# Kernel tuning notes

Hardware: AMD Instinct MI355X
Metric: run time of the kernel (lower is better)

## Reference

```python
import jax, jax.numpy as jnp
import numpy as np

# config (from LLObjectCondensation defaults)
Q_MIN = 0.5
S_B = 1.0
POT_SCALE = 1.0
REP_SCALE = 1.0
BETA_SCALE = 1.0
K_MAX = 128  # max objects per event; truth id 0 == noise


def setup_inputs() -> dict:
    key = jax.random.key(0)
    k1, k2, k3 = jax.random.split(key, 3)
    B, N, C = 8, 40000, 2
    ccoords = jax.random.normal(k1, (B, N, C), dtype=jnp.float32)
    beta = jax.random.uniform(k2, (B, N), dtype=jnp.float32, minval=1e-3, maxval=1.0 - 1e-3)
    t_idx = jax.random.randint(k3, (B, N), 0, K_MAX, dtype=jnp.int32)
    return {"ccoords": ccoords, "beta": beta, "t_idx": t_idx}


def reference(ccoords, beta, t_idx):
    B, N, C = ccoords.shape
    K = K_MAX
    beta_c = jnp.clip(beta, 1e-6, 1.0 - 1e-5)
    # charge q = arctanh^2(beta) + q_min
    q = jnp.arctanh(beta_c / 1.002) ** 2 + Q_MIN  # [B,N]

    obj_ids = jnp.arange(K, dtype=t_idx.dtype)
    M = t_idx[:, :, None] == obj_ids  # [B,N,K] hit-belongs-to-object mask
    is_noise = t_idx == 0  # [B,N]
    obj_present = jnp.any(M, axis=1) & (obj_ids > 0)  # [B,K]

    # condensation point alpha_k = argmax beta among hits of object k
    beta_m = jnp.where(M, beta_c[:, :, None], -1.0)  # [B,N,K]
    alpha = jnp.argmax(beta_m, axis=1)  # [B,K]
    x_alpha = jnp.take_along_axis(
        ccoords, jnp.broadcast_to(alpha[:, :, None], (B, K, C)), axis=1
    )  # [B,K,C]
    q_alpha = jnp.take_along_axis(q, alpha, axis=1)  # [B,K]
    beta_alpha = jnp.take_along_axis(beta_c, alpha, axis=1)  # [B,K]

    # pairwise squared distances hit <-> condensation point, via GEMM form
    xn2 = jnp.sum(ccoords * ccoords, axis=-1)  # [B,N]
    xa2 = jnp.sum(x_alpha * x_alpha, axis=-1)  # [B,K]
    d2 = xn2[:, :, None] + xa2[:, None, :] - 2.0 * jnp.einsum(
        "bnc,bkc->bnk", ccoords, x_alpha
    )
    d2 = jnp.maximum(d2, 0.0)
    d = jnp.sqrt(d2 + 1e-6)

    qq = q[:, :, None] * q_alpha[:, None, :]  # [B,N,K]
    pm = obj_present[:, None, :]
    # attractive: same-object hits pulled to condensation point
    V_attr = jnp.sum(jnp.where(M & pm, d2 * qq, 0.0), axis=(1, 2)) / N  # [B]
    # repulsive: other hits pushed away inside unit radius (hinge)
    V_rep = jnp.sum(
        jnp.where((~M) & pm, jnp.maximum(0.0, 1.0 - d) * qq, 0.0), axis=(1, 2)
    ) / N  # [B]

    n_obj = jnp.maximum(jnp.sum(obj_present, axis=-1), 1)
    L_beta = jnp.sum(jnp.where(obj_present, 1.0 - beta_alpha, 0.0), axis=-1) / n_obj
    n_noise = jnp.maximum(jnp.sum(is_noise, axis=-1), 1)
    L_noise = S_B * jnp.sum(jnp.where(is_noise, beta_c, 0.0), axis=-1) / n_noise

    loss = jnp.mean(
        POT_SCALE * V_attr + REP_SCALE * V_rep + BETA_SCALE * (L_beta + L_noise)
    )
    return loss
```

## Files before the change

### kernel.cpp

```cpp
#include <hip/hip_runtime.h>

#define KOBJ  128
#define QMIN  0.5f
#define SB    1.0f
#define BDIM  256
#define NSCB  128
#define BATCH 8
#define PPB   256


__device__ __forceinline__ float waveRedF(float v) {
    #pragma unroll
    for (int o = 32; o; o >>= 1) v += __shfl_down(v, o, 64);
    return v;
}
__device__ __forceinline__ unsigned int waveRedU(unsigned int v) {
    #pragma unroll
    for (int o = 32; o; o >>= 1) v += __shfl_down(v, o, 64);
    return v;
}

__global__ void __launch_bounds__(BDIM)
oc_scan(const float* __restrict__ beta, const int* __restrict__ t_idx,
        unsigned long long* __restrict__ pkey,
        float* __restrict__ nsp, unsigned int* __restrict__ ncp, int N) {
    const int tid = threadIdx.x;
    const int b   = blockIdx.y;
    const int sub = blockIdx.x;
    const int bid = b * NSCB + sub;
    const int chunk = (N + NSCB - 1) / NSCB;
    const int n0 = sub * chunk;
    const int n1 = min(n0 + chunk, N);

    __shared__ unsigned long long skey[KOBJ];
    if (tid < KOBJ) skey[tid] = 0ull;
    __syncthreads();

    float ns = 0.f;
    unsigned int nc = 0u;
    for (int n = n0 + tid; n < n1; n += BDIM) {
        const float bc = fminf(fmaxf(beta[(size_t)b * N + n], 1e-6f), 1.0f - 1e-5f);
        const int t = t_idx[(size_t)b * N + n];
        const unsigned long long kk =
            ((unsigned long long)__float_as_uint(bc) << 32) |
            (unsigned long long)(~(unsigned int)n);
        atomicMax(&skey[t], kk);
        if (t == 0) { ns += bc; nc++; }
    }
    __syncthreads();
    if (tid < KOBJ) pkey[(size_t)bid * KOBJ + tid] = skey[tid];

    ns = waveRedF(ns);
    nc = waveRedU(nc);
    __shared__ float s_ns[4];
    __shared__ unsigned int s_nc[4];
    if ((tid & 63) == 0) { s_ns[tid >> 6] = ns; s_nc[tid >> 6] = nc; }
    __syncthreads();
    if (tid == 0) {
        float a = 0.f; unsigned int c = 0u;
        #pragma unroll
        for (int w = 0; w < BDIM / 64; ++w) { a += s_ns[w]; c += s_nc[w]; }
        nsp[bid] = a; ncp[bid] = c;
    }
}

__global__ void __launch_bounds__(KOBJ)
oc_reduce(const float* __restrict__ cc,
          const unsigned long long* __restrict__ pkey,
          const float* __restrict__ nsp, const unsigned int* __restrict__ ncp,
          float4* __restrict__ xaq, float* __restrict__ terms, int N) {
    const int b = blockIdx.x;
    const int k = threadIdx.x;

    unsigned long long kv = 0ull;
    #pragma unroll 8
    for (int s = 0; s < NSCB; ++s) {
        const unsigned long long v = pkey[(size_t)(b * NSCB + s) * KOBJ + k];
        kv = v > kv ? v : kv;
    }
    const bool present = (kv != 0ull) && (k > 0);
    float x = 0.f, y = 0.f, qv = 0.f, lb = 0.f;
    unsigned int pc = 0u;
    if (kv != 0ull) {
        const unsigned int na = ~(unsigned int)(kv & 0xFFFFFFFFull);
        const float ba = __uint_as_float((unsigned int)(kv >> 32));
        const float2 xy = *(const float2*)&cc[((size_t)b * N + na) * 2];
        x = xy.x; y = xy.y;
        const float a = atanhf(ba / 1.002f);
        qv = a * a + QMIN;
        if (present) { lb = 1.f - ba; pc = 1u; }
    }
    xaq[(size_t)b * KOBJ + k] = make_float4(x, y, present ? qv : 0.f, 0.f);

    float ns = nsp[b * NSCB + k];
    unsigned int nc = ncp[b * NSCB + k];

    lb = waveRedF(lb);  pc = waveRedU(pc);
    ns = waveRedF(ns);  nc = waveRedU(nc);
    __shared__ float s_lb[2], s_ns2[2];
    __shared__ unsigned int s_pc[2], s_nc2[2];
    const int wv = k >> 6;
    if ((k & 63) == 0) { s_lb[wv] = lb; s_pc[wv] = pc; s_ns2[wv] = ns; s_nc2[wv] = nc; }
    __syncthreads();
    if (k == 0) {
        const float L = s_lb[0] + s_lb[1];
        const unsigned int P = s_pc[0] + s_pc[1];
        const float A = s_ns2[0] + s_ns2[1];
        const unsigned int C = s_nc2[0] + s_nc2[1];
        terms[b] = L / (float)max(P, 1u) + SB * A / (float)max(C, 1u);
    }
}

__global__ void __launch_bounds__(PPB)
oc_pairs(const float* __restrict__ cc, const float* __restrict__ beta,
         const int* __restrict__ t_idx,
         const float4* __restrict__ xaq,
         float* __restrict__ pairp, int N) {
    const int tid = threadIdx.x;
    const int b   = blockIdx.y;
    const int sub = blockIdx.x;
    const int n   = sub * PPB + tid;

    __shared__ float2 sxy[KOBJ];
    __shared__ float  sqv[KOBJ];
    if (tid < KOBJ) {
        const float4 v = xaq[(size_t)b * KOBJ + tid];
        sxy[tid] = make_float2(v.x, v.y);
        sqv[tid] = v.z;
    }
    __syncthreads();

    float acc_tot = 0.f;
    if (n < N) {
        const float2 xy = *(const float2*)&cc[((size_t)b * N + n) * 2];
        const float bc = fminf(fmaxf(beta[(size_t)b * N + n], 1e-6f), 1.0f - 1e-5f);
        const int t = t_idx[(size_t)b * N + n];
        const float a = atanhf(bc / 1.002f);
        const float qn = a * a + QMIN;
        float acc = 0.f;
        #pragma unroll 8
        for (int k = 0; k < KOBJ; ++k) {
            const float dx = xy.x - sxy[k].x;
            const float dy = xy.y - sxy[k].y;
            const float d2 = fmaf(dy, dy, dx * dx);
            const float d = sqrtf(d2 + 1e-6f);
            acc = fmaf(fmaxf(0.f, 1.f - d), sqv[k], acc);
        }
        const float2 st = sxy[t];
        const float dxt = xy.x - st.x;
        const float dyt = xy.y - st.y;
        const float d2t = fmaf(dyt, dyt, dxt * dxt);
        const float dt = sqrtf(d2t + 1e-6f);
        acc += sqv[t] * (d2t - fmaxf(0.f, 1.f - dt));
        acc_tot = acc * qn;
    }

    acc_tot = waveRedF(acc_tot);
    __shared__ float s_acc[PPB / 64];
    if ((tid & 63) == 0) s_acc[tid >> 6] = acc_tot;
    __syncthreads();
    if (tid == 0) {
        float s = 0.f;
        #pragma unroll
        for (int w = 0; w < PPB / 64; ++w) s += s_acc[w];
        pairp[(size_t)b * gridDim.x + sub] = s;
    }
}

__global__ void __launch_bounds__(512)
oc_final(const float* __restrict__ pairp, const float* __restrict__ terms,
         float* __restrict__ out, int N, int nppb) {
    const int tid = threadIdx.x;
    const int total = BATCH * nppb;
    float p = 0.f;
    for (int i = tid; i < total; i += 512) p += pairp[i];
    p = waveRedF(p);
    __shared__ float s_p[8];
    if ((tid & 63) == 0) s_p[tid >> 6] = p;
    __syncthreads();
    if (tid == 0) {
        float P = 0.f;
        #pragma unroll
        for (int w = 0; w < 8; ++w) P += s_p[w];
        float L = 0.f;
        #pragma unroll
        for (int bb = 0; bb < BATCH; ++bb) L += terms[bb];
        out[0] = (P / (float)N + L) / (float)BATCH;
    }
}

extern "C" void kernel_launch(void* const* d_in, const int* in_sizes, int n_in,
                              void* d_out, int out_size, void* d_ws, size_t ws_size,
                              hipStream_t stream) {
    const float* cc   = (const float*)d_in[0];
    const float* beta = (const float*)d_in[1];
    const int*   tid  = (const int*)d_in[2];
    float* out = (float*)d_out;
    const int N = in_sizes[1] / BATCH;

    char* ws = (char*)d_ws;
    unsigned long long* pkey = (unsigned long long*)(ws + 0);
    float*        nsp   = (float*)(ws + 1048576);
    unsigned int* ncp   = (unsigned int*)(ws + 1052672);
    float4*       xaq   = (float4*)(ws + 1056768);
    float*        terms = (float*)(ws + 1073152);
    float*        pairp = (float*)(ws + 1073184);

    const int nppb = (N + PPB - 1) / PPB;

    oc_scan  <<<dim3(NSCB, BATCH), BDIM, 0, stream>>>(beta, tid, pkey, nsp, ncp, N);
    oc_reduce<<<dim3(BATCH), KOBJ, 0, stream>>>(cc, pkey, nsp, ncp, xaq, terms, N);
    oc_pairs <<<dim3(nppb, BATCH), PPB, 0, stream>>>(cc, beta, tid, xaq, pairp, N);
    oc_final <<<dim3(1), 512, 0, stream>>>(pairp, terms, out, N, nppb);
}
```

Before: 43.42 us.

## Fuse final reduction into pairs kernel via last-block counter, simplify hinge loop

Removes the separate oc_final launch. Each pairs block bumps an atomic counter, and the last block to finish reduces all partial sums and the per-batch terms. The inner loop is rewritten algebraically: the sum of max(0,1-d)*q becomes qsum - sum q*min(d,1), with a per-batch qsum computed in the reduce kernel. It also uses the raw hardware sqrt and packs the object table as float4 in shared memory to cut instructions per pair. The trade-off is a threadfence/atomic per block and slightly different rounding from the reformulated sum.

New measurement: 49.08 us. +13.0%, slower.

```diff
diff --git a/kernel.cpp b/kernel.cpp
--- a/kernel.cpp
+++ b/kernel.cpp
@@ -19,11 +19,15 @@
     for (int o = 32; o; o >>= 1) v += __shfl_down(v, o, 64);
     return v;
 }
+__device__ __forceinline__ float agentLoadF(const float* p) {
+    return __hip_atomic_load(p, __ATOMIC_RELAXED, __HIP_MEMORY_SCOPE_AGENT);
+}
 
 __global__ void __launch_bounds__(BDIM)
 oc_scan(const float* __restrict__ beta, const int* __restrict__ t_idx,
         unsigned long long* __restrict__ pkey,
-        float* __restrict__ nsp, unsigned int* __restrict__ ncp, int N) {
+        float* __restrict__ nsp, unsigned int* __restrict__ ncp,
+        unsigned int* __restrict__ ctr, int N) {
     const int tid = threadIdx.x;
     const int b   = blockIdx.y;
     const int sub = blockIdx.x;
@@ -31,6 +35,8 @@
     const int chunk = (N + NSCB - 1) / NSCB;
     const int n0 = sub * chunk;
     const int n1 = min(n0 + chunk, N);
+
+    if (sub == 0 && b == 0 && tid == 0) ctr[0] = 0u;
 
     __shared__ unsigned long long skey[KOBJ];
     if (tid < KOBJ) skey[tid] = 0ull;
@@ -68,7 +74,8 @@
 oc_reduce(const float* __restrict__ cc,
           const unsigned long long* __restrict__ pkey,
           const float* __restrict__ nsp, const unsigned int* __restrict__ ncp,
-          float4* __restrict__ xaq, float* __restrict__ terms, int N) {
+          float4* __restrict__ xaq, float* __restrict__ terms,
+          float* __restrict__ qsum, int N) {
     const int b = blockIdx.x;
     const int k = threadIdx.x;
 
@@ -90,17 +97,20 @@
         qv = a * a + QMIN;
         if (present) { lb = 1.f - ba; pc = 1u; }
     }
-    xaq[(size_t)b * KOBJ + k] = make_float4(x, y, present ? qv : 0.f, 0.f);
+    const float qe = present ? qv : 0.f;
+    xaq[(size_t)b * KOBJ + k] = make_float4(x, y, qe, 0.f);
 
     float ns = nsp[b * NSCB + k];
     unsigned int nc = ncp[b * NSCB + k];
 
+    float qs = qe;
     lb = waveRedF(lb);  pc = waveRedU(pc);
     ns = waveRedF(ns);  nc = waveRedU(nc);
-    __shared__ float s_lb[2], s_ns2[2];
+    qs = waveRedF(qs);
+    __shared__ float s_lb[2], s_ns2[2], s_qs[2];
     __shared__ unsigned int s_pc[2], s_nc2[2];
     const int wv = k >> 6;
-    if ((k & 63) == 0) { s_lb[wv] = lb; s_pc[wv] = pc; s_ns2[wv] = ns; s_nc2[wv] = nc; }
+    if ((k & 63) == 0) { s_lb[wv] = lb; s_pc[wv] = pc; s_ns2[wv] = ns; s_nc2[wv] = nc; s_qs[wv] = qs; }
     __syncthreads();
     if (k == 0) {
         const float L = s_lb[0] + s_lb[1];
@@ -108,6 +118,7 @@
         const float A = s_ns2[0] + s_ns2[1];
         const unsigned int C = s_nc2[0] + s_nc2[1];
         terms[b] = L / (float)max(P, 1u) + SB * A / (float)max(C, 1u);
+        qsum[b]  = s_qs[0] + s_qs[1];
     }
 }
 
@@ -115,19 +126,17 @@
 oc_pairs(const float* __restrict__ cc, const float* __restrict__ beta,
          const int* __restrict__ t_idx,
          const float4* __restrict__ xaq,
-         float* __restrict__ pairp, int N) {
+         const float* __restrict__ terms, const float* __restrict__ qsum,
+         float* __restrict__ pairp, unsigned int* __restrict__ ctr,
+         float* __restrict__ out, int N, int totalPB) {
     const int tid = threadIdx.x;
     const int b   = blockIdx.y;
     const int sub = blockIdx.x;
+    const int bid = b * gridDim.x + sub;
     const int n   = sub * PPB + tid;
 
-    __shared__ float2 sxy[KOBJ];
-    __shared__ float  sqv[KOBJ];
-    if (tid < KOBJ) {
-        const float4 v = xaq[(size_t)b * KOBJ + tid];
-        sxy[tid] = make_float2(v.x, v.y);
-        sqv[tid] = v.z;
-    }
+    __shared__ float4 stab[KOBJ];
+    if (tid < KOBJ) stab[tid] = xaq[(size_t)b * KOBJ + tid];
     __syncthreads();
 
     float acc_tot = 0.f;
@@ -140,52 +149,57 @@
         float acc = 0.f;
         #pragma unroll 8
         for (int k = 0; k < KOBJ; ++k) {
-            const float dx = xy.x - sxy[k].x;
-            const float dy = xy.y - sxy[k].y;
-            const float d2 = fmaf(dy, dy, dx * dx);
-            const float d = sqrtf(d2 + 1e-6f);
-            acc = fmaf(fmaxf(0.f, 1.f - d), sqv[k], acc);
+            const float4 T = stab[k];
+            const float dx = xy.x - T.x;
+            const float dy = xy.y - T.y;
+            const float m   = fmaf(dx, dx, 1e-6f);
+            const float d2e = fmaf(dy, dy, m);
+            const float d   = __builtin_amdgcn_sqrtf(d2e);
+            acc = fmaf(T.z, fminf(d, 1.f), acc);
         }
-        const float2 st = sxy[t];
-        const float dxt = xy.x - st.x;
-        const float dyt = xy.y - st.y;
-        const float d2t = fmaf(dyt, dyt, dxt * dxt);
-        const float dt = sqrtf(d2t + 1e-6f);
-        acc += sqv[t] * (d2t - fmaxf(0.f, 1.f - dt));
-        acc_tot = acc * qn;
+        const float4 Tt = stab[t];
+        const float dxt = xy.x - Tt.x;
+        const float dyt = xy.y - Tt.y;
+        const float mt   = fmaf(dxt, dxt, 1e-6f);
+        const float d2et = fmaf(dyt, dyt, mt);
+        const float dt   = __builtin_amdgcn_sqrtf(d2et);
+        const float point = qsum[b] - acc
+                          + Tt.z * ((d2et - 1e-6f) - 1.f + fminf(dt, 1.f));
+        acc_tot = point * qn;
     }
 
     acc_tot = waveRedF(acc_tot);
     __shared__ float s_acc[PPB / 64];
     if ((tid & 63) == 0) s_acc[tid >> 6] = acc_tot;
     __syncthreads();
+
+    __shared__ int amLast;
     if (tid == 0) {
         float s = 0.f;
         #pragma unroll
         for (int w = 0; w < PPB / 64; ++w) s += s_acc[w];
-        pairp[(size_t)b * gridDim.x + sub] = s;
-    }
-}
-
-__global__ void __launch_bounds__(512)
-oc_final(const float* __restrict__ pairp, const float* __restrict__ terms,
-         float* __restrict__ out, int N, int nppb) {
-    const int tid = threadIdx.x;
-    const int total = BATCH * nppb;
-    float p = 0.f;
-    for (int i = tid; i < total; i += 512) p += pairp[i];
-    p = waveRedF(p);
-    __shared__ float s_p[8];
-    if ((tid & 63) == 0) s_p[tid >> 6] = p;
-    __syncthreads();
-    if (tid == 0) {
-        float P = 0.f;
-        #pragma unroll
-        for (int w = 0; w < 8; ++w) P += s_p[w];
-        float L = 0.f;
-        #pragma unroll
-        for (int bb = 0; bb < BATCH; ++bb) L += terms[bb];
-        out[0] = (P / (float)N + L) / (float)BATCH;
+        pairp[bid] = s;
+        __threadfence();
+        const unsigned int old = atomicAdd(ctr, 1u);
+        amLast = (old == (unsigned int)(totalPB - 1));
+    }
+    __syncthreads();
+
+    if (amLast) {
+        float p = 0.f;
+        for (int i = tid; i < totalPB; i += PPB) p += agentLoadF(&pairp[i]);
+        p = waveRedF(p);
+        __shared__ float s_p[PPB / 64];
+        if ((tid & 63) == 0) s_p[tid >> 6] = p;
+        float t8 = (tid < BATCH) ? agentLoadF(&terms[tid]) : 0.f;
+        t8 = waveRedF(t8);
+        __syncthreads();
+        if (tid == 0) {
+            float P = 0.f;
+            #pragma unroll
+            for (int w = 0; w < PPB / 64; ++w) P += s_p[w];
+            out[0] = (P / (float)N + t8) / (float)BATCH;
+        }
     }
 }
 
@@ -204,12 +218,15 @@
     unsigned int* ncp   = (unsigned int*)(ws + 1052672);
     float4*       xaq   = (float4*)(ws + 1056768);
     float*        terms = (float*)(ws + 1073152);
-    float*        pairp = (float*)(ws + 1073184);
+    float*        qsum  = (float*)(ws + 1073184);
+    float*        pairp = (float*)(ws + 1073216);
+    unsigned int* ctr   = (unsigned int*)(ws + 1078240);
 
     const int nppb = (N + PPB - 1) / PPB;
-
-    oc_scan  <<<dim3(NSCB, BATCH), BDIM, 0, stream>>>(beta, tid, pkey, nsp, ncp, N);
-    oc_reduce<<<dim3(BATCH), KOBJ, 0, stream>>>(cc, pkey, nsp, ncp, xaq, terms, N);
-    oc_pairs <<<dim3(nppb, BATCH), PPB, 0, stream>>>(cc, beta, tid, xaq, pairp, N);
-    oc_final <<<dim3(1), 512, 0, stream>>>(pairp, terms, out, N, nppb);
-}
+    const int totalPB = nppb * BATCH;
+
+    oc_scan  <<<dim3(NSCB, BATCH), BDIM, 0, stream>>>(beta, tid, pkey, nsp, ncp, ctr, N);
+    oc_reduce<<<dim3(BATCH), KOBJ, 0, stream>>>(cc, pkey, nsp, ncp, xaq, terms, qsum, N);
+    oc_pairs <<<dim3(nppb, BATCH), PPB, 0, stream>>>(cc, beta, tid, xaq, terms, qsum,
+                                                     pairp, ctr, out, N, totalPB);
+}
```
